# Optimization experiments

Measured on AMD Instinct MI355X. Metric: run time of the kernel, lower is better.

The kernel has to match this reference:

```python
import jax, jax.numpy as jnp
import numpy as np

DIM = 512
B, QL, KL = 8, 1024, 4096

def setup_inputs() -> dict:
    key = jax.random.key(0)
    k1, k2, k3 = jax.random.split(key, 3)
    output = jax.random.normal(k1, (B, QL, DIM), dtype=jnp.float32)
    context = jax.random.normal(k2, (B, KL, DIM), dtype=jnp.float32)
    # nn.Linear(2*dim, dim): weight [dim, 2*dim]; store transposed [2*dim, dim]
    W_out = jax.random.normal(k3, (DIM, 2 * DIM), dtype=jnp.float32) * (1.0 / np.sqrt(2 * DIM))
    b_out = jnp.zeros((DIM,), dtype=jnp.float32)
    return {"output": output, "context": context, "W_out": W_out, "b_out": b_out}

def reference(output, context, W_out, b_out):
    # scores: [B, QL, KL]
    attn = jnp.einsum("bqd,bkd->bqk", output, context)
    attn = jax.nn.softmax(attn, axis=-1)
    # mix: [B, QL, D]
    mix = jnp.einsum("bqk,bkd->bqd", attn, context)
    combined = jnp.concatenate([mix, output], axis=-1)  # [B, QL, 2D]
    out = jnp.tanh(jnp.einsum("bqe,de->bqd", combined, W_out) + b_out)
    return (out, attn)
```

## Files before the change

### kernel.cpp

```cpp
#include <hip/hip_runtime.h>
#include <math.h>

#define DIMM 512
#define NB 8
#define QLEN 1024
#define KLEN 4096

typedef __attribute__((ext_vector_type(4))) float floatx4;
typedef __attribute__((ext_vector_type(8))) short short8;
typedef __attribute__((ext_vector_type(4))) unsigned short ushort4v;
typedef __attribute__((ext_vector_type(8))) unsigned short ushort8v;

static __device__ __forceinline__ unsigned short f2bf(float f) {
    unsigned u = __builtin_bit_cast(unsigned, f);
    u += 0x7FFFu + ((u >> 16) & 1u);
    return (unsigned short)(u >> 16);
}
static __device__ __forceinline__ float bf2f(unsigned short h) {
    unsigned u = ((unsigned)h) << 16;
    return __builtin_bit_cast(float, u);
}
static __device__ __forceinline__ float fast_tanh(float x) {
    float e = __expf(-2.0f * fabsf(x));
    float t = (1.0f - e) / (1.0f + e);
    return copysignf(t, x);
}

static __device__ __forceinline__ void gload16(const unsigned short* g, unsigned short* l) {
    __builtin_amdgcn_global_load_lds(
        (__attribute__((address_space(1))) void*)const_cast<unsigned short*>(g),
        (__attribute__((address_space(3))) void*)l,
        16, 0, 0);
}

__global__ __launch_bounds__(256) void split_k(const float* __restrict__ x,
                                               unsigned short* __restrict__ dst) {
    int idx = blockIdx.x * 256 + threadIdx.x;
    float4 v = ((const float4*)x)[idx];
    int r = idx >> 7;
    int c = (idx & 127) << 2;
    float f[4] = {v.x, v.y, v.z, v.w};
    ushort4v hi, lo;
#pragma unroll
    for (int e = 0; e < 4; ++e) {
        unsigned short h = f2bf(f[e]);
        hi[e] = h;
        lo[e] = f2bf(f[e] - bf2f(h));
    }
    unsigned short* row = dst + ((size_t)r << 10);
    *(ushort4v*)(row + c) = lo;
    *(ushort4v*)(row + 512 + c) = hi;
}

__global__ __launch_bounds__(256) void conv_hi(const float* __restrict__ x,
                                               unsigned short* __restrict__ dst,
                                               int c4shift, int ldd, int off) {
    int idx = blockIdx.x * 256 + threadIdx.x;
    float4 v = ((const float4*)x)[idx];
    int r = idx >> c4shift;
    int c = (idx & ((1 << c4shift) - 1)) << 2;
    ushort4v hi;
    hi[0] = f2bf(v.x); hi[1] = f2bf(v.y); hi[2] = f2bf(v.z); hi[3] = f2bf(v.w);
    *(ushort4v*)(dst + (size_t)r * ldd + off + c) = hi;
}

__global__ __launch_bounds__(256) void prep_ctx(const float* __restrict__ ctx,
                                                unsigned short* __restrict__ hilo,
                                                unsigned short* __restrict__ ctxT) {
    __shared__ unsigned short tile[64][66];
    int b = blockIdx.z;
    int c0 = blockIdx.x * 64;
    int k0 = blockIdx.y * 64;
    const float* src = ctx + ((size_t)b * KLEN + k0) * DIMM + c0;
    unsigned short* hl = hilo + ((size_t)b * KLEN + k0) * 1024 + c0;
    int t = threadIdx.x;
    int rr = t >> 4, cc4 = (t & 15) * 4;
#pragma unroll
    for (int it = 0; it < 4; ++it) {
        int r = rr + it * 16;
        float4 v = *(const float4*)(src + (size_t)r * DIMM + cc4);
        float f[4] = {v.x, v.y, v.z, v.w};
        ushort4v hi, lo;
#pragma unroll
        for (int e = 0; e < 4; ++e) {
            unsigned short h = f2bf(f[e]);
            hi[e] = h;
            lo[e] = f2bf(f[e] - bf2f(h));
            tile[r][cc4 + e] = h;
        }
        *(ushort4v*)(hl + (size_t)r * 1024 + cc4) = hi;
        *(ushort4v*)(hl + (size_t)r * 1024 + 512 + cc4) = lo;
    }
    __syncthreads();
#pragma unroll
    for (int it = 0; it < 2; ++it) {
        int u = t + it * 256;
        int c = u >> 3;
        int kk = (u & 7) * 8;
        ushort8v o;
#pragma unroll
        for (int e = 0; e < 8; ++e) o[e] = tile[kk + e][c];
        *(ushort8v*)(ctxT + ((size_t)b * DIMM + c0 + c) * KLEN + k0 + kk) = o;
    }
}

__global__ __launch_bounds__(256) void softmax_k(float* __restrict__ S,
                                                 unsigned short* __restrict__ Pb) {
    size_t row = blockIdx.x;
    float* p = S + row * KLEN;
    int t = threadIdx.x;
    int lane = t & 63, wv = t >> 6;
    float4 v[4];
    float mx = -3.0e38f;
#pragma unroll
    for (int i = 0; i < 4; ++i) {
        v[i] = *(const float4*)(p + i * 1024 + t * 4);
        mx = fmaxf(mx, fmaxf(fmaxf(v[i].x, v[i].y), fmaxf(v[i].z, v[i].w)));
    }
#pragma unroll
    for (int m = 32; m >= 1; m >>= 1) mx = fmaxf(mx, __shfl_xor(mx, m, 64));
    __shared__ float redm[4], reds[4];
    if (lane == 0) redm[wv] = mx;
    __syncthreads();
    mx = fmaxf(fmaxf(redm[0], redm[1]), fmaxf(redm[2], redm[3]));
    float sum = 0.f;
#pragma unroll
    for (int i = 0; i < 4; ++i) {
        v[i].x = __expf(v[i].x - mx); v[i].y = __expf(v[i].y - mx);
        v[i].z = __expf(v[i].z - mx); v[i].w = __expf(v[i].w - mx);
        sum += v[i].x + v[i].y + v[i].z + v[i].w;
    }
#pragma unroll
    for (int m = 32; m >= 1; m >>= 1) sum += __shfl_xor(sum, m, 64);
    if (lane == 0) reds[wv] = sum;
    __syncthreads();
    float inv = 1.0f / (reds[0] + reds[1] + reds[2] + reds[3]);
    unsigned short* pb = Pb + row * KLEN;
#pragma unroll
    for (int i = 0; i < 4; ++i) {
        float4 w;
        w.x = v[i].x * inv; w.y = v[i].y * inv; w.z = v[i].z * inv; w.w = v[i].w * inv;
        *(float4*)(p + i * 1024 + t * 4) = w;
        ushort4v h;
        h[0] = f2bf(w.x); h[1] = f2bf(w.y); h[2] = f2bf(w.z); h[3] = f2bf(w.w);
        *(ushort4v*)(pb + i * 1024 + t * 4) = h;
    }
}

template <int EPI, bool REMAP, int BN>
__global__ __launch_bounds__(256, 4) void gemm_bt(
    const unsigned short* __restrict__ A,
    const unsigned short* __restrict__ Bm,
    float* __restrict__ Cf, unsigned short* __restrict__ Cb,
    const float* __restrict__ bias,
    int Ktiles, long lda, long ldb, long ldc,
    long a_bs, long b_bs, long c_bs) {
    constexpr int NF = BN / 32;
    __shared__ unsigned short sA[128 * 64];
    __shared__ unsigned short sB[BN * 64];
    const int tid = threadIdx.x;
    const int lane = tid & 63;
    const int wv = tid >> 6;
    const int wm = wv >> 1, wn = wv & 1;
    const int mlane = lane & 15, quad = lane >> 4;
    const unsigned short* Ab = A + (size_t)blockIdx.z * a_bs + (size_t)blockIdx.y * 128 * lda;
    const unsigned short* Bb = Bm + (size_t)blockIdx.z * b_bs + (size_t)blockIdx.x * BN * ldb;
    const int r8 = tid >> 3;
    const int c8 = (tid & 7) << 3;
    const int cg = ((tid & 7) ^ ((tid >> 3) & 7)) << 3;
    unsigned short* la = sA + r8 * 64 + c8;
    unsigned short* lb = sB + r8 * 64 + c8;

    floatx4 acc[4][NF] = {};

    for (int kt = 0; kt < Ktiles; ++kt) {
        long kv = (long)kt * 64;
        long ka = kv, kb = kv;
        if (REMAP) {
            ka = kv < 512 ? kv + 512 : (kv < 1024 ? kv : kv - 1024);
            kb = kv < 1024 ? kv : kv - 1024;
        }
        if (kt) __syncthreads();
        const unsigned short* ga = Ab + (size_t)r8 * lda + ka + cg;
        const unsigned short* gb = Bb + (size_t)r8 * ldb + kb + cg;
#pragma unroll
        for (int it = 0; it < 4; ++it)
            gload16(ga + (size_t)(it * 32) * lda, la + it * 2048);
#pragma unroll
        for (int it = 0; it < BN / 32; ++it)
            gload16(gb + (size_t)(it * 32) * ldb, lb + it * 2048);
        __syncthreads();
#pragma unroll
        for (int s = 0; s < 2; ++s) {
            const int swz = (((s * 4 + quad) ^ (mlane & 7)) << 3);
            short8 af[4];
#pragma unroll
            for (int i = 0; i < 4; ++i)
                af[i] = *(const short8*)(sA + (wm * 64 + i * 16 + mlane) * 64 + swz);
#pragma unroll
            for (int j = 0; j < NF; ++j) {
                short8 bfj = *(const short8*)(sB + (wn * (BN / 2) + j * 16 + mlane) * 64 + swz);
#pragma unroll
                for (int i = 0; i < 4; ++i)
                    acc[i][j] = __builtin_amdgcn_mfma_f32_16x16x32_bf16(af[i], bfj, acc[i][j], 0, 0, 0);
            }
        }
    }

    size_t crow0 = (size_t)blockIdx.y * 128 + wm * 64 + quad * 4;
    size_t ccol0 = (size_t)blockIdx.x * BN + wn * (BN / 2) + mlane;
    size_t cbase = (size_t)blockIdx.z * c_bs;
#pragma unroll
    for (int i = 0; i < 4; ++i) {
#pragma unroll
        for (int j = 0; j < NF; ++j) {
            size_t gr = crow0 + i * 16;
            size_t gc = ccol0 + j * 16;
#pragma unroll
            for (int r = 0; r < 4; ++r) {
                float vv = acc[i][j][r];
                size_t off = cbase + (gr + r) * ldc + gc;
                if (EPI == 0) Cf[off] = vv;
                else if (EPI == 1) Cb[off] = f2bf(vv);
                else Cf[off] = fast_tanh(vv + bias[gc]);
            }
        }
    }
}

extern "C" void kernel_launch(void* const* d_in, const int* in_sizes, int n_in,
                              void* d_out, int out_size, void* d_ws, size_t ws_size,
                              hipStream_t stream) {
    (void)in_sizes; (void)n_in; (void)out_size; (void)ws_size;
    const float* outp = (const float*)d_in[0];
    const float* ctx  = (const float*)d_in[1];
    const float* W    = (const float*)d_in[2];
    const float* bias = (const float*)d_in[3];

    float* out0 = (float*)d_out;
    float* attn = out0 + (size_t)NB * QLEN * DIMM;

    unsigned char* w = (unsigned char*)d_ws;
    unsigned short* R1 = (unsigned short*)(w);
    unsigned short* R2 = (unsigned short*)(w + (16ull << 20));
    unsigned short* R3 = (unsigned short*)(w + (80ull << 20));
    unsigned short* R4 = (unsigned short*)(w + (112ull << 20));

    split_k<<<4096, 256, 0, stream>>>(outp, R1);
    prep_ctx<<<dim3(8, 64, 8), 256, 0, stream>>>(ctx, R2, R3);
    conv_hi<<<512, 256, 0, stream>>>(W, R4, 8, 1024, 0);

    gemm_bt<0, true, 128><<<dim3(32, 8, 8), 256, 0, stream>>>(
        R1, R2, attn, nullptr, nullptr,
        24, 1024, 1024, 4096,
        (long)QLEN * 1024, (long)KLEN * 1024, (long)QLEN * KLEN);

    softmax_k<<<8192, 256, 0, stream>>>(attn, R2);

    gemm_bt<1, false, 64><<<dim3(8, 8, 8), 256, 0, stream>>>(
        R2, R3, nullptr, R1, nullptr,
        64, 4096, 4096, 1024,
        (long)QLEN * KLEN, (long)DIMM * KLEN, (long)QLEN * 1024);

    gemm_bt<2, false, 64><<<dim3(8, 64, 1), 256, 0, stream>>>(
        R1, R4, out0, nullptr, bias,
        16, 1024, 1024, 512, 0, 0, 0);
}
```

Baseline: 469.9 us.

## Double-buffer LDS tiles in bf16 GEMM to overlap global loads with MFMA

```diff
diff --git a/kernel.cpp b/kernel.cpp
--- a/kernel.cpp
+++ b/kernel.cpp
@@ -148,7 +148,7 @@
 }
 
 template <int EPI, bool REMAP, int BN>
-__global__ __launch_bounds__(256, 4) void gemm_bt(
+__global__ __launch_bounds__(256, 2) void gemm_bt(
     const unsigned short* __restrict__ A,
     const unsigned short* __restrict__ Bm,
     float* __restrict__ Cf, unsigned short* __restrict__ Cb,
@@ -156,8 +156,9 @@
     int Ktiles, long lda, long ldb, long ldc,
     long a_bs, long b_bs, long c_bs) {
     constexpr int NF = BN / 32;
-    __shared__ unsigned short sA[128 * 64];
-    __shared__ unsigned short sB[BN * 64];
+    constexpr int NLOADS = 4 + BN / 32;
+    __shared__ unsigned short sA[2][128 * 64];
+    __shared__ unsigned short sB[2][BN * 64];
     const int tid = threadIdx.x;
     const int lane = tid & 63;
     const int wv = tid >> 6;
@@ -168,43 +169,63 @@
     const int r8 = tid >> 3;
     const int c8 = (tid & 7) << 3;
     const int cg = ((tid & 7) ^ ((tid >> 3) & 7)) << 3;
-    unsigned short* la = sA + r8 * 64 + c8;
-    unsigned short* lb = sB + r8 * 64 + c8;
 
     floatx4 acc[4][NF] = {};
 
-    for (int kt = 0; kt < Ktiles; ++kt) {
+    auto stage = [&](int b, int kt) {
         long kv = (long)kt * 64;
         long ka = kv, kb = kv;
         if (REMAP) {
             ka = kv < 512 ? kv + 512 : (kv < 1024 ? kv : kv - 1024);
             kb = kv < 1024 ? kv : kv - 1024;
         }
-        if (kt) __syncthreads();
         const unsigned short* ga = Ab + (size_t)r8 * lda + ka + cg;
         const unsigned short* gb = Bb + (size_t)r8 * ldb + kb + cg;
+        unsigned short* la = sA[b] + r8 * 64 + c8;
+        unsigned short* lb = sB[b] + r8 * 64 + c8;
 #pragma unroll
         for (int it = 0; it < 4; ++it)
             gload16(ga + (size_t)(it * 32) * lda, la + it * 2048);
 #pragma unroll
         for (int it = 0; it < BN / 32; ++it)
             gload16(gb + (size_t)(it * 32) * ldb, lb + it * 2048);
-        __syncthreads();
+    };
+
+    stage(0, 0);
+    asm volatile("s_waitcnt vmcnt(0)" ::: "memory");
+    __builtin_amdgcn_s_barrier();
+
+    int cur = 0;
+    for (int kt = 0; kt < Ktiles; ++kt) {
+        if (kt + 1 < Ktiles) {
+            stage(cur ^ 1, kt + 1);
+            if constexpr (NLOADS == 8)
+                asm volatile("s_waitcnt vmcnt(8)" ::: "memory");
+            else
+                asm volatile("s_waitcnt vmcnt(6)" ::: "memory");
+        } else {
+            asm volatile("s_waitcnt vmcnt(0)" ::: "memory");
+        }
+        __builtin_amdgcn_s_barrier();
+        const unsigned short* pA = sA[cur];
+        const unsigned short* pB = sB[cur];
 #pragma unroll
         for (int s = 0; s < 2; ++s) {
             const int swz = (((s * 4 + quad) ^ (mlane & 7)) << 3);
             short8 af[4];
 #pragma unroll
             for (int i = 0; i < 4; ++i)
-                af[i] = *(const short8*)(sA + (wm * 64 + i * 16 + mlane) * 64 + swz);
+                af[i] = *(const short8*)(pA + (wm * 64 + i * 16 + mlane) * 64 + swz);
 #pragma unroll
             for (int j = 0; j < NF; ++j) {
-                short8 bfj = *(const short8*)(sB + (wn * (BN / 2) + j * 16 + mlane) * 64 + swz);
+                short8 bfj = *(const short8*)(pB + (wn * (BN / 2) + j * 16 + mlane) * 64 + swz);
 #pragma unroll
                 for (int i = 0; i < 4; ++i)
                     acc[i][j] = __builtin_amdgcn_mfma_f32_16x16x32_bf16(af[i], bfj, acc[i][j], 0, 0, 0);
             }
         }
+        __builtin_amdgcn_s_barrier();
+        cur ^= 1;
     }
 
     size_t crow0 = (size_t)blockIdx.y * 128 + wm * 64 + quad * 4;
```

Result: slower. 490.0 us (+4.3%).
